# Kernel tuning notes

Measured on AMD Instinct MI355X. Metric: run time of the kernel, lower is better.

## Reference

```python
import jax, jax.numpy as jnp
import numpy as np

TRI_TABLE = np.array([[-1,-1,-1,-1,-1,-1],[1,0,2,-1,-1,-1],[4,0,3,-1,-1,-1],[1,4,2,1,3,4],[3,1,5,-1,-1,-1],[2,3,0,2,5,3],[1,4,0,1,5,4],[4,2,5,-1,-1,-1],[4,5,2,-1,-1,-1],[4,1,0,4,5,1],[3,2,0,3,5,2],[1,3,5,-1,-1,-1],[4,1,2,4,3,1],[3,0,4,-1,-1,-1],[2,0,1,-1,-1,-1],[-1,-1,-1,-1,-1,-1]], dtype=np.int64)
NUM_TRI_TABLE = np.array([0,1,1,2,1,2,2,1,1,2,2,1,2,1,1,0], dtype=np.int64)
BASE_TET_EDGES = np.array([0,1,0,2,0,3,1,2,1,3,2,3], dtype=np.int64)
GRID_RES = 128  # -> 12,582,912 tets, 2,146,689 grid vertices (matches 128_tets.npz scale)


def _grid_tets(G):
    # Regular G^3 cube grid in [-1,1]^3; each cube split into 6 tets around the 0-7 diagonal.
    V = G + 1
    lin = np.linspace(-1.0, 1.0, V, dtype=np.float32)
    zz, yy, xx = np.meshgrid(lin, lin, lin, indexing='ij')
    pos = np.stack([xx, yy, zz], axis=-1).reshape(-1, 3)
    idx = np.arange(V ** 3, dtype=np.int64).reshape(V, V, V)
    c = lambda dz, dy, dx: idx[dz:dz + G, dy:dy + G, dx:dx + G].ravel()
    corners = np.stack([c(0,0,0), c(0,0,1), c(0,1,0), c(0,1,1), c(1,0,0), c(1,0,1), c(1,1,0), c(1,1,1)], axis=1)
    six = np.array([[0,5,1,7],[0,1,3,7],[0,3,2,7],[0,2,6,7],[0,6,4,7],[0,4,5,7]], dtype=np.int64)
    tets = corners[:, six].reshape(-1, 4)
    return pos, tets


def setup_inputs():
    pos, tets = _grid_tets(GRID_RES)
    # Sphere SDF (radius 0.5) -> realistic thin shell of surface-crossing tets.
    sdf = (0.5 - np.linalg.norm(pos, axis=-1)).astype(np.float32)
    return {"pos_nx3": jnp.asarray(pos), "sdf_n": jnp.asarray(sdf), "tet_fx4": jnp.asarray(tets)}


def _index_pipeline(sdf_np, tet_np):
    # Non-differentiable, data-dependent-shape part (torch.no_grad block in the original).
    occ = sdf_np > 0
    occ4 = occ[tet_np]                                   # [F,4]
    occ_sum = occ4.sum(-1)
    valid = (occ_sum > 0) & (occ_sum < 4)                # tets crossed by the iso-surface
    edges = tet_np[valid][:, BASE_TET_EDGES].reshape(-1, 2)
    edges = np.sort(edges, axis=1)                       # sort_edges
    unique_edges, idx_map = np.unique(edges, axis=0, return_inverse=True)
    mask_edges = occ[unique_edges].sum(-1) == 1          # edges with a sign change
    mapping = np.full(unique_edges.shape[0], -1, dtype=np.int64)
    mapping[mask_edges] = np.arange(mask_edges.sum(), dtype=np.int64)
    idx_map = mapping[idx_map.reshape(-1)].reshape(-1, 6)
    interp_v = unique_edges[mask_edges]                  # [E,2] endpoints to interpolate
    tetindex = (occ4[valid] * np.array([1, 2, 4, 8], dtype=np.int64)).sum(-1)
    num_tri = NUM_TRI_TABLE[tetindex]
    return valid, idx_map, interp_v, tetindex, num_tri


def _faces_and_uv(valid, idx_map, tetindex, num_tri, num_tets):
    m1, m2 = num_tri == 1, num_tri == 2
    f1 = np.take_along_axis(idx_map[m1], TRI_TABLE[tetindex[m1]][:, :3], axis=1).reshape(-1, 3)
    f2 = np.take_along_axis(idx_map[m2], TRI_TABLE[tetindex[m2]][:, :6], axis=1).reshape(-1, 3)
    faces = np.concatenate([f1, f2], axis=0)
    tet_gidx = np.arange(num_tets, dtype=np.int64)[valid]
    face_gidx = np.concatenate([tet_gidx[m1] * 2,
                                np.stack([tet_gidx[m2] * 2, tet_gidx[m2] * 2 + 1], axis=-1).reshape(-1)], axis=0)
    max_idx = num_tets * 2
    N = int(np.ceil(np.sqrt((max_idx + 1) // 2)))
    lin = np.linspace(0.0, 1.0 - 1.0 / N, N, dtype=np.float32)
    ty, tx = np.meshgrid(lin, lin, indexing='ij')        # torch.meshgrid default 'ij'
    pad = np.float32(0.9 / N)
    uvs = np.stack([tx, ty, tx + pad, ty, tx + pad, ty + pad, tx, ty + pad], axis=-1).reshape(-1, 2)
    tet_idx = face_gidx // 2
    tet_idx = (tet_idx // N) * N + (tet_idx % N)
    tri_idx = face_gidx % 2
    uv_idx = np.stack([tet_idx * 4, tet_idx * 4 + tri_idx + 1, tet_idx * 4 + tri_idx + 2], axis=-1)
    return faces, uvs, uv_idx


def reference(pos_nx3, sdf_n, tet_fx4):
    tet_np = np.asarray(tet_fx4)
    sdf_np = np.asarray(sdf_n)
    valid, idx_map, interp_v, tetindex, num_tri = _index_pipeline(sdf_np, tet_np)
    # Differentiable part: linear interpolation of crossing vertices along sign-change edges.
    iv = jnp.asarray(interp_v.reshape(-1))
    p = pos_nx3[iv].reshape(-1, 2, 3)                    # [E,2,3]
    s = sdf_n[iv].reshape(-1, 2)                         # [E,2]
    denom = s[:, 0] - s[:, 1]                            # s0 + (-s1), as in the original
    w = jnp.stack([-s[:, 1], s[:, 0]], axis=-1) / denom[:, None]  # flip([s0,-s1]) / denom
    verts = (p * w[:, :, None]).sum(axis=1)              # [E,3]
    faces, uvs, uv_idx = _faces_and_uv(valid, idx_map, tetindex, num_tri, tet_np.shape[0])
    return verts, jnp.asarray(faces), jnp.asarray(uvs), jnp.asarray(uv_idx)
```

## Files before the change

### kernel.cpp

```cpp
#include <hip/hip_runtime.h>
#include <cmath>

typedef unsigned int u32;
typedef unsigned long long u64;
typedef unsigned char u8;
typedef unsigned short u16;
typedef float f32x4 __attribute__((ext_vector_type(4)));

__constant__ signed char c_tri[16][6] = {
    {-1,-1,-1,-1,-1,-1},
    { 1, 0, 2,-1,-1,-1},
    { 4, 0, 3,-1,-1,-1},
    { 1, 4, 2, 1, 3, 4},
    { 3, 1, 5,-1,-1,-1},
    { 2, 3, 0, 2, 5, 3},
    { 1, 4, 0, 1, 5, 4},
    { 4, 2, 5,-1,-1,-1},
    { 4, 5, 2,-1,-1,-1},
    { 4, 1, 0, 4, 5, 1},
    { 3, 2, 0, 3, 5, 2},
    { 1, 3, 5,-1,-1,-1},
    { 4, 1, 2, 4, 3, 1},
    { 3, 0, 4,-1,-1,-1},
    { 2, 0, 1,-1,-1,-1},
    {-1,-1,-1,-1,-1,-1}};
__constant__ signed char c_ntri[16] = {0,1,1,2,1,2,2,1,1,2,2,1,2,1,1,0};
__constant__ signed char c_edge_p[6] = {0,0,0,1,1,2};
__constant__ signed char c_edge_q[6] = {1,2,3,2,3,3};
__constant__ u8 c_six[6][4] = {{0,5,1,7},{0,1,3,7},{0,3,2,7},{0,2,6,7},{0,6,4,7},{0,4,5,7}};

__global__ void k_main(const float* __restrict__ sdf, u8* __restrict__ vmask,
                       u16* __restrict__ pfx16, u32* __restrict__ vbsums,
                       u32* __restrict__ cbsums, int Nv, int V, int G) {
    int v = blockIdx.x * 256 + threadIdx.x;
    u32 cnt = 0, pack = 0;
    if (v < Nv) {
        int x = v % V;
        int t = v / V;
        int y = t % V;
        int z = t / V;
        const int V2 = V * V;
        float s0 = sdf[v];
        bool occ0 = s0 > 0.0f;
        bool bx = x < G, by = y < G, bz = z < G;
        int  d[7]  = {1, V, V + 1, V2, V2 + 1, V2 + V, V2 + V + 1};
        bool ok[7] = {bx, by, bx && by, bz, bx && bz, by && bz, bx && by && bz};
        u32 m = 0;
        u32 occ8 = occ0 ? 1u : 0u;
#pragma unroll
        for (int k = 0; k < 7; ++k) {
            if (ok[k]) {
                bool o1 = sdf[v + d[k]] > 0.0f;
                occ8 |= (u32)o1 << (k + 1);
                if (o1 != occ0) m |= (1u << k);
            }
        }
        vmask[v] = (u8)(m | (occ0 ? 0x80u : 0u));
        cnt = __popc(m);
        if (bx && by && bz) {
            u32 c1 = 0, c2 = 0;
#pragma unroll
            for (int w = 0; w < 6; ++w) {
                int ti = ((occ8 >> c_six[w][0]) & 1) | (((occ8 >> c_six[w][1]) & 1) << 1) |
                         (((occ8 >> c_six[w][2]) & 1) << 2) | (((occ8 >> c_six[w][3]) & 1) << 3);
                int nt = c_ntri[ti];
                c1 += (nt == 1);
                c2 += (nt == 2);
            }
            pack = c1 | (c2 << 16);
        }
    }
    int lane = threadIdx.x & 63, wid = threadIdx.x >> 6;
    u32 s = cnt, sp = pack;
#pragma unroll
    for (int o = 1; o < 64; o <<= 1) {
        u32 t = __shfl_up(s, o, 64);
        u32 tp = __shfl_up(sp, o, 64);
        if (lane >= o) { s += t; sp += tp; }
    }
    __shared__ u32 wsum[4], wpk[4];
    if (lane == 63) { wsum[wid] = s; wpk[wid] = sp; }
    __syncthreads();
    u32 wb = 0;
#pragma unroll
    for (int k = 0; k < 4; ++k)
        if (k < wid) wb += wsum[k];
    if (v < Nv) pfx16[v] = (u16)(wb + s - cnt);
    if (threadIdx.x == 0) {
        vbsums[blockIdx.x] = wsum[0] + wsum[1] + wsum[2] + wsum[3];
        cbsums[blockIdx.x] = wpk[0] + wpk[1] + wpk[2] + wpk[3];
    }
}

__global__ void k_scan_both(u32* __restrict__ vbsums, int nV,
                            const u32* __restrict__ cbsums, u64* __restrict__ coffs,
                            int nC, u32* __restrict__ totals) {
    int tid = threadIdx.x;
    int lane = tid & 63, wid = tid >> 6;
    if (blockIdx.x == 0) {
        __shared__ u32 wsum[16];
        __shared__ u32 carry;
        if (tid == 0) carry = 0;
        __syncthreads();
        for (int start = 0; start < nV; start += 4096) {
            int i0 = start + tid * 4;
            u32 a0 = (i0     < nV) ? vbsums[i0]     : 0u;
            u32 a1 = (i0 + 1 < nV) ? vbsums[i0 + 1] : 0u;
            u32 a2 = (i0 + 2 < nV) ? vbsums[i0 + 2] : 0u;
            u32 a3 = (i0 + 3 < nV) ? vbsums[i0 + 3] : 0u;
            u32 t1 = a0 + a1, t2 = t1 + a2, t3 = t2 + a3;
            u32 v = t3;
#pragma unroll
            for (int o = 1; o < 64; o <<= 1) {
                u32 t = __shfl_up(v, o, 64);
                if (lane >= o) v += t;
            }
            if (lane == 63) wsum[wid] = v;
            __syncthreads();
            if (wid == 0) {
                u32 w = (lane < 16) ? wsum[lane] : 0u;
#pragma unroll
                for (int o = 1; o < 16; o <<= 1) {
                    u32 t = __shfl_up(w, o, 64);
                    if (lane >= o) w += t;
                }
                if (lane < 16) wsum[lane] = w;
            }
            __syncthreads();
            u32 eb = carry + (wid ? wsum[wid - 1] : 0u) + v - t3;
            if (i0     < nV) vbsums[i0]     = eb;
            if (i0 + 1 < nV) vbsums[i0 + 1] = eb + a0;
            if (i0 + 2 < nV) vbsums[i0 + 2] = eb + t1;
            if (i0 + 3 < nV) vbsums[i0 + 3] = eb + t2;
            __syncthreads();
            if (tid == 0) carry += wsum[15];
            __syncthreads();
        }
        if (tid == 0) totals[0] = carry;
    } else {
        __shared__ u64 wsum[16];
        __shared__ u64 carry;
        if (tid == 0) carry = 0;
        __syncthreads();
        for (int start = 0; start < nC; start += 4096) {
            int i0 = start + tid * 4;
            u32 r0 = (i0     < nC) ? cbsums[i0]     : 0u;
            u32 r1 = (i0 + 1 < nC) ? cbsums[i0 + 1] : 0u;
            u32 r2 = (i0 + 2 < nC) ? cbsums[i0 + 2] : 0u;
            u32 r3 = (i0 + 3 < nC) ? cbsums[i0 + 3] : 0u;
            u64 a0 = (u64)(r0 & 0xFFFFu) | ((u64)(r0 >> 16) << 32);
            u64 a1 = (u64)(r1 & 0xFFFFu) | ((u64)(r1 >> 16) << 32);
            u64 a2 = (u64)(r2 & 0xFFFFu) | ((u64)(r2 >> 16) << 32);
            u64 a3 = (u64)(r3 & 0xFFFFu) | ((u64)(r3 >> 16) << 32);
            u64 t1 = a0 + a1, t2 = t1 + a2, t3 = t2 + a3;
            u64 v = t3;
#pragma unroll
            for (int o = 1; o < 64; o <<= 1) {
                u64 t = __shfl_up(v, o, 64);
                if (lane >= o) v += t;
            }
            if (lane == 63) wsum[wid] = v;
            __syncthreads();
            if (wid == 0) {
                u64 w = (lane < 16) ? wsum[lane] : 0ull;
#pragma unroll
                for (int o = 1; o < 16; o <<= 1) {
                    u64 t = __shfl_up(w, o, 64);
                    if (lane >= o) w += t;
                }
                if (lane < 16) wsum[lane] = w;
            }
            __syncthreads();
            u64 eb = carry + (wid ? wsum[wid - 1] : 0ull) + v - t3;
            if (i0     < nC) coffs[i0]     = eb;
            if (i0 + 1 < nC) coffs[i0 + 1] = eb + a0;
            if (i0 + 2 < nC) coffs[i0 + 2] = eb + t1;
            if (i0 + 3 < nC) coffs[i0 + 3] = eb + t2;
            __syncthreads();
            if (tid == 0) carry += wsum[15];
            __syncthreads();
        }
        if (tid == 0) {
            totals[1] = (u32)(carry & 0xFFFFFFFFull);
            totals[2] = (u32)(carry >> 32);
        }
    }
}

__device__ inline float uv_elem(long long e, int Nuv, double invN, double step_d,
                                float pad, float last) {
    int p = (int)(e >> 3);
    int i = (int)((double)p * invN);
    int j = p - i * Nuv;
    if (j >= Nuv) { j -= Nuv; ++i; }
    int r = (int)(e & 7);
    int c = r >> 1;
    if ((r & 1) == 0) {
        float tx = (j == Nuv - 1) ? last : (float)((double)j * step_d);
        return tx + ((c == 1 || c == 2) ? pad : 0.0f);
    }
    float ty = (i == Nuv - 1) ? last : (float)((double)i * step_d);
    return ty + ((c >= 2) ? pad : 0.0f);
}

__global__ void k_tail(const float* __restrict__ sdf, const u8* __restrict__ vmask,
                       const u16* __restrict__ pfx16, const u32* __restrict__ vbsums,
                       const u64* __restrict__ coffs, const u32* __restrict__ totals,
                       float* __restrict__ out, int Nv, int V, int G, int nbV,
                       float h, int Nuv, double invN, double step_d, float pad,
                       float last, long long npts2) {
    int tid = threadIdx.x;
    int b0 = blockIdx.x;
    int nfront = 2 * nbV;
    int fidx = -1;
    if (b0 % 6 == 0) {
        int f = b0 / 6;
        if (f < nfront) fidx = f;
    }
    if (fidx >= 0 && fidx < nbV) {
        int b = fidx;
        int v = b * 256 + tid;
        const int V2 = V * V;
        u32 pack = 0, occ8 = 0;
        int x = 0, y = 0, z = 0;
        bool interior = false;
        if (v < Nv) {
            x = v % V;
            int t = v / V;
            y = t % V;
            z = t / V;
            interior = (x < G) && (y < G) && (z < G);
        }
        const int off[8] = {0, 1, V, V + 1, V2, V2 + 1, V2 + V, V2 + V + 1};
        if (interior) {
#pragma unroll
            for (int n = 0; n < 8; ++n) occ8 |= (u32)(vmask[v + off[n]] >> 7) << n;
            u32 c1 = 0, c2 = 0;
#pragma unroll
            for (int w = 0; w < 6; ++w) {
                int ti = ((occ8 >> c_six[w][0]) & 1) | (((occ8 >> c_six[w][1]) & 1) << 1) |
                         (((occ8 >> c_six[w][2]) & 1) << 2) | (((occ8 >> c_six[w][3]) & 1) << 3);
                int nt = c_ntri[ti];
                c1 += (nt == 1);
                c2 += (nt == 2);
            }
            pack = c1 | (c2 << 16);
        }
        int lane = tid & 63, wid = tid >> 6;
        u32 s = pack;
#pragma unroll
        for (int o = 1; o < 64; o <<= 1) {
            u32 t = __shfl_up(s, o, 64);
            if (lane >= o) s += t;
        }
        __shared__ u32 wsum[4];
        if (lane == 63) wsum[wid] = s;
        __syncthreads();
        u32 wb = 0;
#pragma unroll
        for (int k = 0; k < 4; ++k)
            if (k < wid) wb += wsum[k];
        u32 excl = wb + s - pack;
        if (!interior || pack == 0) return;

        u64 bo = coffs[b];
        u32 m1pos = (u32)(bo & 0xFFFFFFFFull) + (excl & 0xFFFFu);
        u32 m2pos = (u32)(bo >> 32) + (excl >> 16);
        u32 E = totals[0], Tm1 = totals[1], Tm2 = totals[2];
        u64 T = (u64)Tm1 + 2ull * (u64)Tm2;
        float* faces = out + 3ull * E;
        float* uvidx = out + 3ull * E + 3ull * T + (u64)npts2;
        int ci = (z * G + y) * G + x;

#pragma unroll
        for (int w = 0; w < 6; ++w) {
            int ti = ((occ8 >> c_six[w][0]) & 1) | (((occ8 >> c_six[w][1]) & 1) << 1) |
                     (((occ8 >> c_six[w][2]) & 1) << 2) | (((occ8 >> c_six[w][3]) & 1) << 3);
            int nt = c_ntri[ti];
            if (!nt) continue;
            int t = ci * 6 + w;
            for (int tri = 0; tri < nt; ++tri) {
                u64 r = (nt == 1) ? (u64)m1pos : ((u64)Tm1 + 2ull * (u64)m2pos + (u64)tri);
#pragma unroll
                for (int cidx = 0; cidx < 3; ++cidx) {
                    int e = c_tri[ti][3 * tri + cidx];
                    int np_ = c_six[w][(int)c_edge_p[e]];
                    int nq_ = c_six[w][(int)c_edge_q[e]];
                    int lo = np_ < nq_ ? np_ : nq_;
                    int k = (np_ ^ nq_) - 1;
                    int lonode = v + off[lo];
                    u32 vi = vbsums[lonode >> 8] + (u32)pfx16[lonode] +
                             (u32)__popc((u32)(vmask[lonode] & 0x7Fu) & ((1u << k) - 1u));
                    faces[3ull * r + cidx] = (float)vi;
                }
                uvidx[3ull * r + 0] = (float)(4 * t);
                uvidx[3ull * r + 1] = (float)(4 * t + tri + 1);
                uvidx[3ull * r + 2] = (float)(4 * t + tri + 2);
            }
            if (nt == 1) m1pos++;
            else m2pos++;
        }
        return;
    }
    if (fidx >= 0) {
        int vb = fidx - nbV;
        int v = vb * 256 + tid;
        if (v >= Nv) return;
        u32 m = (u32)(vmask[v] & 0x7Fu);
        if (!m) return;
        u32 r = vbsums[vb] + (u32)pfx16[v];
        int x = v % V;
        int t2 = v / V;
        int y = t2 % V;
        int z = t2 / V;
        const int V2 = V * V;
        const int d[7]  = {1, V, V + 1, V2, V2 + 1, V2 + V, V2 + V + 1};
        const int dx[7] = {1, 0, 1, 0, 1, 0, 1};
        const int dy[7] = {0, 1, 1, 0, 0, 1, 1};
        const int dz[7] = {0, 0, 0, 1, 1, 1, 1};
        float px = -1.0f + x * h, py = -1.0f + y * h, pz = -1.0f + z * h;
        float s0 = sdf[v];
#pragma unroll
        for (int k = 0; k < 7; ++k) {
            if (m & (1u << k)) {
                float s1 = sdf[v + d[k]];
                float denom = s0 - s1;
                float w0 = -s1 / denom;
                float w1 = s0 / denom;
                out[3ull * r + 0] = px * w0 + (px + dx[k] * h) * w1;
                out[3ull * r + 1] = py * w0 + (py + dy[k] * h) * w1;
                out[3ull * r + 2] = pz * w0 + (pz + dz[k] * h) * w1;
                r++;
            }
        }
        return;
    }
    int uidx = b0 - min((b0 + 5) / 6, nfront);
    u32 E = totals[0], Tm1 = totals[1], Tm2 = totals[2];
    u64 base = 3ull * E + 3ull * ((u64)Tm1 + 2ull * (u64)Tm2);
    float* uvs = out + base;
    long long head = (long long)((4 - (base & 3)) & 3);
    long long nvec = (npts2 - head) >> 2;
    long long t = (long long)uidx * 256 + tid;
    if (t < nvec) {
        long long e0 = head + 4 * t;
        int p = (int)(e0 >> 3);
        int i = (int)((double)p * invN);
        int j = p - i * Nuv;
        if (j >= Nuv) { j -= Nuv; ++i; }
        float tx = (j == Nuv - 1) ? last : (float)((double)j * step_d);
        float ty = (i == Nuv - 1) ? last : (float)((double)i * step_d);
        f32x4 vals;
        int pcur = p;
#pragma unroll
        for (int q = 0; q < 4; ++q) {
            long long e = e0 + q;
            int pe = (int)(e >> 3);
            if (pe != pcur) {
                pcur = pe;
                ++j;
                if (j == Nuv) {
                    j = 0;
                    ++i;
                    ty = (i == Nuv - 1) ? last : (float)((double)i * step_d);
                }
                tx = (j == Nuv - 1) ? last : (float)((double)j * step_d);
            }
            int r = (int)(e & 7);
            int c = r >> 1;
            float vv;
            if ((r & 1) == 0) vv = tx + ((c == 1 || c == 2) ? pad : 0.0f);
            else              vv = ty + ((c >= 2) ? pad : 0.0f);
            vals[q] = vv;
        }
        __builtin_nontemporal_store(vals, (f32x4*)(uvs + e0));
    } else if (t == nvec) {
        for (long long e = 0; e < head; ++e)
            uvs[e] = uv_elem(e, Nuv, invN, step_d, pad, last);
        for (long long e = head + 4 * nvec; e < npts2; ++e)
            uvs[e] = uv_elem(e, Nuv, invN, step_d, pad, last);
    }
}

extern "C" void kernel_launch(void* const* d_in, const int* in_sizes, int n_in,
                              void* d_out, int out_size, void* d_ws, size_t ws_size,
                              hipStream_t stream) {
    const float* sdf = (const float*)d_in[1];
    int Nv = in_sizes[1];
    int F = in_sizes[2] / 4;

    int V = 1;
    while ((long long)V * V * V < (long long)Nv) V++;
    int G = V - 1;

    long long half = (2ll * (long long)F + 1) / 2;
    int Nuv = (int)std::sqrt((double)half);
    while ((long long)Nuv * Nuv < half) Nuv++;
    while (Nuv > 1 && (long long)(Nuv - 1) * (Nuv - 1) >= half) Nuv--;

    int nbV = (Nv + 255) / 256;
    long long npts2 = 2ll * 4ll * (long long)Nuv * (long long)Nuv;

    double invN = 1.0 / (double)Nuv;
    double step_d = (1.0 - invN) / (double)(Nuv - 1);
    float pad = (float)(0.9 * invN);
    float last = (float)(1.0 - invN);

    char* ws = (char*)d_ws;
    size_t off = 0;
    auto walloc = [&](size_t bytes) -> void* {
        void* p = ws + off;
        off = (off + bytes + 255) & ~(size_t)255;
        return p;
    };
    u32* totals = (u32*)walloc(64);
    u32* vbsums = (u32*)walloc(sizeof(u32) * (size_t)nbV);
    u32* cbsums = (u32*)walloc(sizeof(u32) * (size_t)nbV);
    u64* coffs  = (u64*)walloc(sizeof(u64) * (size_t)nbV);
    u8*  vmask  = (u8*)walloc((size_t)Nv);
    u16* pfx16  = (u16*)walloc(sizeof(u16) * (size_t)Nv);
    (void)ws_size;

    float* out = (float*)d_out;
    float h = 2.0f / (float)G;

    long long nthr_uvs = npts2 / 4 + 1;
    int nbU = (int)((nthr_uvs + 255) / 256);
    int nfront = 2 * nbV;
    int nbTail = nbU + nfront;

    hipLaunchKernelGGL(k_main, dim3(nbV), dim3(256), 0, stream, sdf, vmask, pfx16, vbsums,
                       cbsums, Nv, V, G);
    hipLaunchKernelGGL(k_scan_both, dim3(2), dim3(1024), 0, stream, vbsums, nbV, cbsums, coffs,
                       nbV, totals);
    hipLaunchKernelGGL(k_tail, dim3(nbTail), dim3(256), 0, stream, sdf, vmask, pfx16,
                       vbsums, coffs, totals, out, Nv, V, G, nbV, h, Nuv, invN, step_d, pad,
                       last, npts2);
}
```

Baseline: 147.6 us.

## Replace serial block-sum scan with coarse group scan plus per-block local reductions

The two-block sequential scan over per-block sums is replaced by a single-block kernel that sums groups of 33 block totals and scans only those group sums. Each consumer block in the tail kernel then rebuilds its exact block offsets by a wave reduction over at most 32 entries of its group, caching the needed neighbour-block prefixes in shared memory. This shortens the latency-bound middle kernel, at the cost of extra loads, reductions and a block barrier in every tail block.

```diff
diff --git a/kernel.cpp b/kernel.cpp
--- a/kernel.cpp
+++ b/kernel.cpp
@@ -6,6 +6,8 @@
 typedef unsigned char u8;
 typedef unsigned short u16;
 typedef float f32x4 __attribute__((ext_vector_type(4)));
+
+#define GS 33
 
 __constant__ signed char c_tri[16][6] = {
     {-1,-1,-1,-1,-1,-1},
@@ -92,99 +94,68 @@
     }
 }
 
-__global__ void k_scan_both(u32* __restrict__ vbsums, int nV,
-                            const u32* __restrict__ cbsums, u64* __restrict__ coffs,
-                            int nC, u32* __restrict__ totals) {
+__global__ void k_mid(const u32* __restrict__ vbsums, const u32* __restrict__ cbsums,
+                      int nbV, u32* __restrict__ coarseV, u64* __restrict__ coarseC,
+                      u32* __restrict__ totals) {
     int tid = threadIdx.x;
     int lane = tid & 63, wid = tid >> 6;
-    if (blockIdx.x == 0) {
-        __shared__ u32 wsum[16];
-        __shared__ u32 carry;
-        if (tid == 0) carry = 0;
-        __syncthreads();
-        for (int start = 0; start < nV; start += 4096) {
-            int i0 = start + tid * 4;
-            u32 a0 = (i0     < nV) ? vbsums[i0]     : 0u;
-            u32 a1 = (i0 + 1 < nV) ? vbsums[i0 + 1] : 0u;
-            u32 a2 = (i0 + 2 < nV) ? vbsums[i0 + 2] : 0u;
-            u32 a3 = (i0 + 3 < nV) ? vbsums[i0 + 3] : 0u;
-            u32 t1 = a0 + a1, t2 = t1 + a2, t3 = t2 + a3;
-            u32 v = t3;
-#pragma unroll
-            for (int o = 1; o < 64; o <<= 1) {
-                u32 t = __shfl_up(v, o, 64);
-                if (lane >= o) v += t;
-            }
-            if (lane == 63) wsum[wid] = v;
-            __syncthreads();
-            if (wid == 0) {
-                u32 w = (lane < 16) ? wsum[lane] : 0u;
-#pragma unroll
-                for (int o = 1; o < 16; o <<= 1) {
-                    u32 t = __shfl_up(w, o, 64);
-                    if (lane >= o) w += t;
-                }
-                if (lane < 16) wsum[lane] = w;
-            }
-            __syncthreads();
-            u32 eb = carry + (wid ? wsum[wid - 1] : 0u) + v - t3;
-            if (i0     < nV) vbsums[i0]     = eb;
-            if (i0 + 1 < nV) vbsums[i0 + 1] = eb + a0;
-            if (i0 + 2 < nV) vbsums[i0 + 2] = eb + t1;
-            if (i0 + 3 < nV) vbsums[i0 + 3] = eb + t2;
-            __syncthreads();
-            if (tid == 0) carry += wsum[15];
-            __syncthreads();
-        }
-        if (tid == 0) totals[0] = carry;
-    } else {
-        __shared__ u64 wsum[16];
-        __shared__ u64 carry;
-        if (tid == 0) carry = 0;
-        __syncthreads();
-        for (int start = 0; start < nC; start += 4096) {
-            int i0 = start + tid * 4;
-            u32 r0 = (i0     < nC) ? cbsums[i0]     : 0u;
-            u32 r1 = (i0 + 1 < nC) ? cbsums[i0 + 1] : 0u;
-            u32 r2 = (i0 + 2 < nC) ? cbsums[i0 + 2] : 0u;
-            u32 r3 = (i0 + 3 < nC) ? cbsums[i0 + 3] : 0u;
-            u64 a0 = (u64)(r0 & 0xFFFFu) | ((u64)(r0 >> 16) << 32);
-            u64 a1 = (u64)(r1 & 0xFFFFu) | ((u64)(r1 >> 16) << 32);
-            u64 a2 = (u64)(r2 & 0xFFFFu) | ((u64)(r2 >> 16) << 32);
-            u64 a3 = (u64)(r3 & 0xFFFFu) | ((u64)(r3 >> 16) << 32);
-            u64 t1 = a0 + a1, t2 = t1 + a2, t3 = t2 + a3;
-            u64 v = t3;
-#pragma unroll
-            for (int o = 1; o < 64; o <<= 1) {
-                u64 t = __shfl_up(v, o, 64);
-                if (lane >= o) v += t;
-            }
-            if (lane == 63) wsum[wid] = v;
-            __syncthreads();
-            if (wid == 0) {
-                u64 w = (lane < 16) ? wsum[lane] : 0ull;
-#pragma unroll
-                for (int o = 1; o < 16; o <<= 1) {
-                    u64 t = __shfl_up(w, o, 64);
-                    if (lane >= o) w += t;
-                }
-                if (lane < 16) wsum[lane] = w;
-            }
-            __syncthreads();
-            u64 eb = carry + (wid ? wsum[wid - 1] : 0ull) + v - t3;
-            if (i0     < nC) coffs[i0]     = eb;
-            if (i0 + 1 < nC) coffs[i0 + 1] = eb + a0;
-            if (i0 + 2 < nC) coffs[i0 + 2] = eb + t1;
-            if (i0 + 3 < nC) coffs[i0 + 3] = eb + t2;
-            __syncthreads();
-            if (tid == 0) carry += wsum[15];
-            __syncthreads();
-        }
-        if (tid == 0) {
-            totals[1] = (u32)(carry & 0xFFFFFFFFull);
-            totals[2] = (u32)(carry >> 32);
-        }
-    }
+    int NG = (nbV + GS - 1) / GS;
+    u32 gv = 0;
+    u64 gc = 0;
+    if (tid < NG) {
+        int s0 = tid * GS;
+        int e0 = s0 + GS;
+        if (e0 > nbV) e0 = nbV;
+        for (int i = s0; i < e0; ++i) {
+            gv += vbsums[i];
+            u32 rc = cbsums[i];
+            gc += (u64)(rc & 0xFFFFu) | ((u64)(rc >> 16) << 32);
+        }
+    }
+    u32 v = gv;
+    u64 c = gc;
+#pragma unroll
+    for (int o = 1; o < 64; o <<= 1) {
+        u32 tv = __shfl_up(v, o, 64);
+        u64 tc = __shfl_up(c, o, 64);
+        if (lane >= o) { v += tv; c += tc; }
+    }
+    __shared__ u32 wsV[16];
+    __shared__ u64 wsC[16];
+    if (lane == 63) { wsV[wid] = v; wsC[wid] = c; }
+    __syncthreads();
+    if (wid == 0) {
+        u32 wv = (lane < 16) ? wsV[lane] : 0u;
+        u64 wc = (lane < 16) ? wsC[lane] : 0ull;
+#pragma unroll
+        for (int o = 1; o < 16; o <<= 1) {
+            u32 tv = __shfl_up(wv, o, 64);
+            u64 tc = __shfl_up(wc, o, 64);
+            if (lane >= o) { wv += tv; wc += tc; }
+        }
+        if (lane < 16) { wsV[lane] = wv; wsC[lane] = wc; }
+    }
+    __syncthreads();
+    u32 ebv = (wid ? wsV[wid - 1] : 0u) + v - gv;
+    u64 ebc = (wid ? wsC[wid - 1] : 0ull) + c - gc;
+    if (tid < NG) { coarseV[tid] = ebv; coarseC[tid] = ebc; }
+    if (tid == NG - 1) {
+        totals[0] = ebv + gv;
+        u64 tc = ebc + gc;
+        totals[1] = (u32)(tc & 0xFFFFFFFFull);
+        totals[2] = (u32)(tc >> 32);
+    }
+}
+
+__device__ inline u32 vpfx_wave(const u32* __restrict__ vbsums,
+                                const u32* __restrict__ coarseV, int k, int ln) {
+    int g0 = k / GS;
+    int rem = k - g0 * GS;
+    u32 part = (ln < rem) ? vbsums[g0 * GS + ln] : 0u;
+#pragma unroll
+    for (int o = 32; o > 0; o >>= 1) part += __shfl_down(part, o, 64);
+    u32 r = coarseV[g0] + part;
+    return r;
 }
 
 __device__ inline float uv_elem(long long e, int Nuv, double invN, double step_d,
@@ -205,7 +176,8 @@
 
 __global__ void k_tail(const float* __restrict__ sdf, const u8* __restrict__ vmask,
                        const u16* __restrict__ pfx16, const u32* __restrict__ vbsums,
-                       const u64* __restrict__ coffs, const u32* __restrict__ totals,
+                       const u32* __restrict__ cbsums, const u32* __restrict__ coarseV,
+                       const u64* __restrict__ coarseC, const u32* __restrict__ totals,
                        float* __restrict__ out, int Nv, int V, int G, int nbV,
                        float h, int Nuv, double invN, double step_d, float pad,
                        float last, long long npts2) {
@@ -261,11 +233,41 @@
         for (int k = 0; k < 4; ++k)
             if (k < wid) wb += wsum[k];
         u32 excl = wb + s - pack;
+
+        __shared__ u32 sh_vpfx[5];
+        __shared__ u32 sh_bo_lo, sh_bo_hi;
+        int K = V2 >> 8;
+        if (wid < 4) {
+            int koff = (wid == 0) ? 0 : (wid == 1) ? 1 : (wid == 2) ? K : K + 1;
+            int k = b + koff;
+            u32 r = 0;
+            if (k < nbV) r = vpfx_wave(vbsums, coarseV, k, lane);
+            if (lane == 0) sh_vpfx[wid] = r;
+            if (wid == 3) {
+                int k2 = b + K + 2;
+                u32 r2 = 0;
+                if (k2 < nbV) r2 = vpfx_wave(vbsums, coarseV, k2, lane);
+                if (lane == 0) sh_vpfx[4] = r2;
+            }
+            if (wid == 0) {
+                int g0 = b / GS;
+                int rem = b - g0 * GS;
+                u32 rc = (lane < rem) ? cbsums[g0 * GS + lane] : 0u;
+                u64 part = (u64)(rc & 0xFFFFu) | ((u64)(rc >> 16) << 32);
+#pragma unroll
+                for (int o = 32; o > 0; o >>= 1) part += __shfl_down(part, o, 64);
+                if (lane == 0) {
+                    u64 bo = coarseC[g0] + part;
+                    sh_bo_lo = (u32)(bo & 0xFFFFFFFFull);
+                    sh_bo_hi = (u32)(bo >> 32);
+                }
+            }
+        }
+        __syncthreads();
         if (!interior || pack == 0) return;
 
-        u64 bo = coffs[b];
-        u32 m1pos = (u32)(bo & 0xFFFFFFFFull) + (excl & 0xFFFFu);
-        u32 m2pos = (u32)(bo >> 32) + (excl >> 16);
+        u32 m1pos = sh_bo_lo + (excl & 0xFFFFu);
+        u32 m2pos = sh_bo_hi + (excl >> 16);
         u32 E = totals[0], Tm1 = totals[1], Tm2 = totals[2];
         u64 T = (u64)Tm1 + 2ull * (u64)Tm2;
         float* faces = out + 3ull * E;
@@ -289,7 +291,10 @@
                     int lo = np_ < nq_ ? np_ : nq_;
                     int k = (np_ ^ nq_) - 1;
                     int lonode = v + off[lo];
-                    u32 vi = vbsums[lonode >> 8] + (u32)pfx16[lonode] +
+                    int d0 = (lonode >> 8) - b;
+                    int sel = (d0 == 0) ? 0 : (d0 == 1) ? 1 : (d0 == K) ? 2
+                              : (d0 == K + 1) ? 3 : 4;
+                    u32 vi = sh_vpfx[sel] + (u32)pfx16[lonode] +
                              (u32)__popc((u32)(vmask[lonode] & 0x7Fu) & ((1u << k) - 1u));
                     faces[3ull * r + cidx] = (float)vi;
                 }
@@ -304,11 +309,20 @@
     }
     if (fidx >= 0) {
         int vb = fidx - nbV;
+        __shared__ u32 sh_vbase;
+        {
+            int lane = tid & 63, wid = tid >> 6;
+            if (wid == 0) {
+                u32 r = vpfx_wave(vbsums, coarseV, vb, lane);
+                if (lane == 0) sh_vbase = r;
+            }
+        }
+        __syncthreads();
         int v = vb * 256 + tid;
         if (v >= Nv) return;
         u32 m = (u32)(vmask[v] & 0x7Fu);
         if (!m) return;
-        u32 r = vbsums[vb] + (u32)pfx16[v];
+        u32 r = sh_vbase + (u32)pfx16[v];
         int x = v % V;
         int t2 = v / V;
         int y = t2 % V;
@@ -413,12 +427,13 @@
         off = (off + bytes + 255) & ~(size_t)255;
         return p;
     };
-    u32* totals = (u32*)walloc(64);
-    u32* vbsums = (u32*)walloc(sizeof(u32) * (size_t)nbV);
-    u32* cbsums = (u32*)walloc(sizeof(u32) * (size_t)nbV);
-    u64* coffs  = (u64*)walloc(sizeof(u64) * (size_t)nbV);
-    u8*  vmask  = (u8*)walloc((size_t)Nv);
-    u16* pfx16  = (u16*)walloc(sizeof(u16) * (size_t)Nv);
+    u32* totals  = (u32*)walloc(64);
+    u32* vbsums  = (u32*)walloc(sizeof(u32) * (size_t)nbV);
+    u32* cbsums  = (u32*)walloc(sizeof(u32) * (size_t)nbV);
+    u32* coarseV = (u32*)walloc(sizeof(u32) * 1024);
+    u64* coarseC = (u64*)walloc(sizeof(u64) * 1024);
+    u8*  vmask   = (u8*)walloc((size_t)Nv);
+    u16* pfx16   = (u16*)walloc(sizeof(u16) * (size_t)Nv);
     (void)ws_size;
 
     float* out = (float*)d_out;
@@ -431,9 +446,9 @@
 
     hipLaunchKernelGGL(k_main, dim3(nbV), dim3(256), 0, stream, sdf, vmask, pfx16, vbsums,
                        cbsums, Nv, V, G);
-    hipLaunchKernelGGL(k_scan_both, dim3(2), dim3(1024), 0, stream, vbsums, nbV, cbsums, coffs,
-                       nbV, totals);
+    hipLaunchKernelGGL(k_mid, dim3(1), dim3(1024), 0, stream, vbsums, cbsums, nbV, coarseV,
+                       coarseC, totals);
     hipLaunchKernelGGL(k_tail, dim3(nbTail), dim3(256), 0, stream, sdf, vmask, pfx16,
-                       vbsums, coffs, totals, out, Nv, V, G, nbV, h, Nuv, invN, step_d, pad,
-                       last, npts2);
-}
+                       vbsums, cbsums, coarseV, coarseC, totals, out, Nv, V, G, nbV, h, Nuv,
+                       invN, step_d, pad, last, npts2);
+}
```

New measurement: 165.7 us. 1.12x slower.
